# Performance work log

Measured on AMD Instinct MI355X. Metric: run time of the kernel, lower is better.

The kernel has to match this reference:

```python
import jax, jax.numpy as jnp
import numpy as np

INF = 1000000000.0
D = 1024


def setup_inputs() -> dict:
    key = jax.random.key(0)
    k_enc, k_r = jax.random.split(key)
    encoding = jax.random.normal(k_enc, (8, 2048, D), dtype=jnp.float32)
    R = jax.random.normal(k_r, (D, D), dtype=jnp.float32) / D  # init_with_zeros=False
    return {"encoding": encoding, "R": R}


def reference(encoding, R):
    b, n, d = encoding.shape
    # Q = encoding @ R ; scores = Q @ encoding^T  (bilinear relation attention)
    encR = jnp.einsum("bnd,de->bne", encoding, R)          # [b, n, d]
    scores = jnp.einsum("bnd,bmd->bnm", encR, encoding)     # [b, n, n]
    # causal mask: -INF above the diagonal (use_mask=True)
    mask = jnp.where(jnp.tril(jnp.ones((n, n), dtype=bool)), 0.0, -INF).astype(scores.dtype)
    A = jax.nn.softmax(scores + mask, axis=2)               # [b, n, n]
    return jnp.einsum("bnm,bmd->bnd", A, encoding)          # [b, n, d]
```

## Files before the change

kernel.cpp:

```cpp
#include <hip/hip_runtime.h>
#include <hip/hip_bf16.h>


typedef __attribute__((ext_vector_type(4))) float f32x4;
typedef __attribute__((ext_vector_type(4))) unsigned u32x4;
typedef __attribute__((ext_vector_type(8))) __fp16 f16x8;
typedef __attribute__((ext_vector_type(4))) __fp16 f16x4;
typedef __attribute__((ext_vector_type(2))) __fp16 f16x2;

#define MFMA16H(A, B, C) __builtin_amdgcn_mfma_f32_16x16x32_f16(A, B, C, 0, 0, 0)

__device__ __forceinline__ f16x4 cvt4h(f32x4 a) {
    union { f16x4 v; f16x2 h[2]; } r;
    r.h[0] = __builtin_amdgcn_cvt_pkrtz(a[0], a[1]);
    r.h[1] = __builtin_amdgcn_cvt_pkrtz(a[2], a[3]);
    return r.v;
}

__device__ __forceinline__ void gload16(const void* g, void* l) {
    __builtin_amdgcn_global_load_lds(
        (const __attribute__((address_space(1))) unsigned*)g,
        (__attribute__((address_space(3))) unsigned*)l, 16, 0, 0);
}

#define BAR() do { __builtin_amdgcn_sched_barrier(0); \
                   __builtin_amdgcn_s_barrier();      \
                   __builtin_amdgcn_sched_barrier(0); } while (0)

__global__ __launch_bounds__(256) void transpose_cvt_kernel(
    const float* __restrict__ enc, __fp16* __restrict__ encT, __fp16* __restrict__ encH,
    const float* __restrict__ R, __fp16* __restrict__ Rt)
{
    __shared__ __align__(16) char lt[64 * 128];
    const int t = threadIdx.x;
    const int bz = blockIdx.z;
    const bool isR = (bz == 8);
    if (isR && blockIdx.x >= 16) return;
    const int Rr = isR ? 1024 : 2048, C = 1024;
    const float* src = isR ? R : enc;
    __fp16* dstT = isR ? Rt : encT;
    __fp16* dstH = isR ? (__fp16*)nullptr : encH;
    const int r0 = blockIdx.x * 64, c0 = blockIdx.y * 64;
    const size_t so = isR ? 0 : (size_t)bz * Rr * C;
    const int tr = t >> 4;
    const int tc4 = (t & 15) * 4;
#pragma unroll
    for (int p = 0; p < 4; ++p) {
        int rl = tr + 16 * p;
        f32x4 x = *(const f32x4*)(src + so + (size_t)(r0 + rl) * C + c0 + tc4);
        f16x4 h = cvt4h(x);
        if (dstH) *(f16x4*)(dstH + so + (size_t)(r0 + rl) * C + c0 + tc4) = h;
        *(f16x4*)(lt + rl * 128 + ((tc4 * 2) ^ ((rl & 7) << 4))) = h;
    }
    __syncthreads();
#pragma unroll
    for (int p = 0; p < 4; ++p) {
        int dl = tr + 16 * p;
#pragma unroll
        for (int j = 0; j < 4; ++j) {
            int kl = (t & 15) + 16 * j;
            __fp16 v = *(const __fp16*)(lt + kl * 128 + ((dl * 2) ^ ((kl & 7) << 4)));
            dstT[so + (size_t)(c0 + dl) * Rr + r0 + kl] = v;
        }
    }
}

__global__ __launch_bounds__(512, 2) void gemm_qr256(
    const __fp16* __restrict__ encH, const __fp16* __restrict__ Rt,
    __fp16* __restrict__ Qh)
{
    __shared__ __align__(16) char lds[131072];
    const int t = threadIdx.x;
    const int w = t >> 6, l = t & 63;
    const int l15 = l & 15, lg = (l >> 4) & 3;
    const int wr = w >> 2, wc = w & 3;
    const int bm = ((int)blockIdx.x >> 2) * 256;
    const int bn = ((int)blockIdx.x & 3) * 256;
    const __fp16* Ag = encH + (size_t)bm * 1024;
    const __fp16* Bg = Rt + (size_t)bn * 1024;

    const int srow = 32 * w + (l >> 2);
    const int slg = ((l & 3) - ((l >> 3) & 3)) & 3;
    const int slotr = ((l >> 4) + ((l & 15) >> 1)) & 3;

    f32x4 acc[8][4];
#pragma unroll
    for (int i = 0; i < 8; ++i)
#pragma unroll
        for (int j = 0; j < 4; ++j) acc[i][j] = (f32x4){0.f, 0.f, 0.f, 0.f};

    auto stage = [&](int op, int tile, int kh) {
        const __fp16* src = (op ? Bg : Ag) + (size_t)srow * 1024 + tile * 64 + kh * 32 + slg * 8;
        char* dst = lds + (tile & 1) * 65536 + op * 32768 + kh * 16384 + w * 2048;
        gload16(src, dst);
        gload16(src + (size_t)16 * 1024, dst + 1024);
    };
    auto rdA = [&](int buf, int ks, int mf) {
        return *(const f16x8*)(lds + buf * 65536 + ks * 16384
                               + (128 * wr + 16 * mf + l15) * 64 + slotr * 16);
    };
    auto rdB = [&](int buf, int ks, int nf) {
        return *(const f16x8*)(lds + buf * 65536 + 32768 + ks * 16384
                               + (64 * wc + 16 * nf + l15) * 64 + slotr * 16);
    };

    stage(0, 0, 0); stage(1, 0, 0); stage(0, 0, 1); stage(1, 0, 1);
    stage(0, 1, 0); stage(1, 1, 0);

    f16x8 afr[4], bfr[4];

#define MF16(mbase)                                                     \
    __builtin_amdgcn_s_setprio(1);                                      \
    _Pragma("unroll") for (int mf = 0; mf < 4; ++mf)                    \
        _Pragma("unroll") for (int nf = 0; nf < 4; ++nf)                \
            acc[(mbase) + mf][nf] = MFMA16H(afr[mf], bfr[nf], acc[(mbase) + mf][nf]); \
    __builtin_amdgcn_s_setprio(0);

    for (int i = 0; i < 8; ++i) {
        const bool lastI = (i == 7);
        asm volatile("s_waitcnt vmcnt(8)" ::: "memory");
        BAR();
#pragma unroll
        for (int nf = 0; nf < 4; ++nf) bfr[nf] = rdB(0, 0, nf);
#pragma unroll
        for (int mf = 0; mf < 4; ++mf) afr[mf] = rdA(0, 0, mf);
        stage(0, 2 * i + 1, 1);
        MF16(0)
        BAR();
#pragma unroll
        for (int mf = 0; mf < 4; ++mf) afr[mf] = rdA(0, 0, mf + 4);
        stage(1, 2 * i + 1, 1);
        MF16(4)
        asm volatile("s_waitcnt vmcnt(8)" ::: "memory");
        BAR();
#pragma unroll
        for (int nf = 0; nf < 4; ++nf) bfr[nf] = rdB(0, 1, nf);
#pragma unroll
        for (int mf = 0; mf < 4; ++mf) afr[mf] = rdA(0, 1, mf);
        if (!lastI) stage(0, 2 * i + 2, 0);
        MF16(0)
        BAR();
#pragma unroll
        for (int mf = 0; mf < 4; ++mf) afr[mf] = rdA(0, 1, mf + 4);
        if (!lastI) stage(1, 2 * i + 2, 0);
        MF16(4)
        if (!lastI) asm volatile("s_waitcnt vmcnt(8)" ::: "memory");
        else        asm volatile("s_waitcnt vmcnt(4)" ::: "memory");
        BAR();
#pragma unroll
        for (int nf = 0; nf < 4; ++nf) bfr[nf] = rdB(1, 0, nf);
#pragma unroll
        for (int mf = 0; mf < 4; ++mf) afr[mf] = rdA(1, 0, mf);
        if (!lastI) stage(0, 2 * i + 2, 1);
        MF16(0)
        BAR();
#pragma unroll
        for (int mf = 0; mf < 4; ++mf) afr[mf] = rdA(1, 0, mf + 4);
        if (!lastI) stage(1, 2 * i + 2, 1);
        MF16(4)
        if (!lastI) asm volatile("s_waitcnt vmcnt(8)" ::: "memory");
        else        asm volatile("s_waitcnt vmcnt(0)" ::: "memory");
        BAR();
#pragma unroll
        for (int nf = 0; nf < 4; ++nf) bfr[nf] = rdB(1, 1, nf);
#pragma unroll
        for (int mf = 0; mf < 4; ++mf) afr[mf] = rdA(1, 1, mf);
        if (!lastI) stage(0, 2 * i + 3, 0);
        MF16(0)
        BAR();
#pragma unroll
        for (int mf = 0; mf < 4; ++mf) afr[mf] = rdA(1, 1, mf + 4);
        if (!lastI) stage(1, 2 * i + 3, 0);
        MF16(4)
    }
#undef MF16

#pragma unroll
    for (int mf = 0; mf < 8; ++mf)
#pragma unroll
        for (int nf = 0; nf < 4; ++nf)
#pragma unroll
            for (int rg = 0; rg < 4; ++rg) {
                int rr = bm + 128 * wr + 16 * mf + 4 * lg + rg;
                int cc = bn + 64 * wc + 16 * nf + l15;
                Qh[(size_t)rr * 1024 + cc] = (__fp16)acc[mf][nf][rg];
            }
}

template <int CMODE>
__device__ __forceinline__ void core256x128(
    const __fp16* __restrict__ A, int ldA, const __fp16* __restrict__ B, int ldB,
    char* __restrict__ Cptr, int ldC, int K, int rowOff, int colOff, bool maskDiag)
{
    __shared__ __align__(16) char lds[73728];
    const int t = threadIdx.x;
    const int w = t >> 6, l = t & 63;
    const int l15 = l & 15, lg = (l >> 4) & 3;
    const int wr = w >> 1, wc = w & 1;

    const int srowA = 32 * w + (l >> 2);
    const int srowB = 16 * w + (l >> 2);
    const int slg = ((l & 3) - ((l >> 3) & 3)) & 3;
    const int slotr = ((l >> 4) + ((l & 15) >> 1)) & 3;

    f32x4 acc[4][4];
#pragma unroll
    for (int i = 0; i < 4; ++i)
#pragma unroll
        for (int j = 0; j < 4; ++j) acc[i][j] = (f32x4){0.f, 0.f, 0.f, 0.f};
    f32x4 acc_rs[4];
#pragma unroll
    for (int i = 0; i < 4; ++i) acc_rs[i] = (f32x4){0.f, 0.f, 0.f, 0.f};
    f16x8 ones;
#pragma unroll
    for (int j = 0; j < 8; ++j) ones[j] = (__fp16)1.f;

    auto stageH = [&](int h) {
        const int reg = h % 3;
        const __fp16* sa = A + (size_t)srowA * ldA + h * 32 + slg * 8;
        char* da = lds + reg * 16384 + w * 2048;
        gload16(sa, da);
        gload16(sa + (size_t)16 * ldA, da + 1024);
        const __fp16* sb = B + (size_t)srowB * ldB + h * 32 + slg * 8;
        gload16(sb, lds + 49152 + reg * 8192 + w * 1024);
    };
    auto rdA = [&](int h, int mf) {
        return *(const f16x8*)(lds + (h % 3) * 16384
                               + (64 * wr + 16 * mf + l15) * 64 + slotr * 16);
    };
    auto rdB = [&](int h, int nf) {
        return *(const f16x8*)(lds + 49152 + (h % 3) * 8192
                               + (64 * wc + 16 * nf + l15) * 64 + slotr * 16);
    };

    const int nh = K >> 5;
    stageH(0); stageH(1);

    f16x8 afr[4], bfr[4];
    for (int h = 0; h < nh; ++h) {
        if (h + 1 < nh) asm volatile("s_waitcnt vmcnt(3)" ::: "memory");
        else            asm volatile("s_waitcnt vmcnt(0)" ::: "memory");
        BAR();
#pragma unroll
        for (int nf = 0; nf < 4; ++nf) bfr[nf] = rdB(h, nf);
#pragma unroll
        for (int mf = 0; mf < 4; ++mf) afr[mf] = rdA(h, mf);
        if (h + 2 < nh) stageH(h + 2);
        __builtin_amdgcn_s_setprio(1);
#pragma unroll
        for (int mf = 0; mf < 4; ++mf) {
#pragma unroll
            for (int nf = 0; nf < 4; ++nf)
                acc[mf][nf] = MFMA16H(afr[mf], bfr[nf], acc[mf][nf]);
            if (CMODE == 2)
                acc_rs[mf] = MFMA16H(afr[mf], ones, acc_rs[mf]);
        }
        __builtin_amdgcn_s_setprio(0);
    }
    BAR();

    if (CMODE == 1) {
#pragma unroll
        for (int mf = 0; mf < 4; ++mf)
#pragma unroll
            for (int nf = 0; nf < 4; ++nf)
#pragma unroll
                for (int rg = 0; rg < 4; ++rg) {
                    int rr = 64 * wr + 16 * mf + 4 * lg + rg;
                    int cc = 64 * wc + 16 * nf + l15;
                    bool msk = maskDiag && (colOff + cc > rowOff + rr);
                    float e = msk ? 0.f
                                  : __builtin_amdgcn_exp2f(acc[mf][nf][rg] * 1.4426950408889634f);
                    *(__fp16*)(Cptr + ((size_t)rr * ldC + cc) * 2) = (__fp16)e;
                }
    } else {
#pragma unroll
        for (int mf = 0; mf < 4; ++mf)
#pragma unroll
            for (int nf = 0; nf < 4; ++nf)
#pragma unroll
                for (int rg = 0; rg < 4; ++rg) {
                    int rr = 64 * wr + 16 * mf + 4 * lg + rg;
                    int cc = 64 * wc + 16 * nf + l15;
                    *(float*)(Cptr + ((size_t)rr * ldC + cc) * 4) =
                        acc[mf][nf][rg] / acc_rs[mf][rg];
                }
    }
}

__global__ __launch_bounds__(512, 4) void gemm_s256(
    const __fp16* __restrict__ Qh, const __fp16* __restrict__ encH,
    __fp16* __restrict__ S)
{
    const int b = (int)blockIdx.x & 7;
    const int r = (int)blockIdx.x >> 3;
    int qt = 0;
    while (r >= (qt + 1) * (qt + 2)) ++qt;
    const int nt = r - qt * (qt + 1);
    const size_t bo = (size_t)b * 2048 * 1024;
    const size_t so = (size_t)b * 2048 * 2048;
    core256x128<1>(Qh + bo + (size_t)(256 * qt) * 1024, 1024,
                   encH + bo + (size_t)(128 * nt) * 1024, 1024,
                   (char*)(S + so + (size_t)(256 * qt) * 2048 + 128 * nt), 2048,
                   1024, 256 * qt, 128 * nt, (nt >> 1) == qt);
}

__global__ __launch_bounds__(512, 4) void gemm_pv256(
    const __fp16* __restrict__ P, const __fp16* __restrict__ encT,
    float* __restrict__ out)
{
    const int b = (int)blockIdx.x & 7;
    const int r = (int)blockIdx.x >> 3;
    const int qtb = 7 - (r >> 3);
    const int dblk = r & 7;
    const size_t so = (size_t)b * 2048 * 2048;
    const size_t to = (size_t)b * 1024 * 2048;
    const size_t oo = (size_t)b * 2048 * 1024;
    core256x128<2>(P + so + (size_t)(256 * qtb) * 2048, 2048,
                   encT + to + (size_t)(128 * dblk) * 2048, 2048,
                   (char*)(out + oo + (size_t)(256 * qtb) * 1024 + 128 * dblk), 1024,
                   256 * (qtb + 1), 0, 0, false);
}

__global__ __launch_bounds__(256) void softmax_kernel(__fp16* __restrict__ S, int sh)
{
    const int t = threadIdx.x;
    const int wv = t >> 6, l = t & 63;
    const int r = blockIdx.x * 4 + wv;
    const int b = blockIdx.y;
    __fp16* row = S + ((size_t)b * 2048 + r) * 2048;
    const int L = ((r >> sh) + 1) << sh;

    float v[4][8];
    float mx = -1e30f;
#pragma unroll
    for (int i = 0; i < 4; ++i) {
        int c0 = 8 * l + 512 * i;
        if (c0 < L) {
            f16x8 h = *reinterpret_cast<const f16x8*>(row + c0);
#pragma unroll
            for (int j = 0; j < 8; ++j) { v[i][j] = (float)h[j]; mx = fmaxf(mx, v[i][j]); }
        } else {
#pragma unroll
            for (int j = 0; j < 8; ++j) v[i][j] = -1e30f;
        }
    }
#pragma unroll
    for (int off = 1; off < 64; off <<= 1) mx = fmaxf(mx, __shfl_xor(mx, off));
    float sm = 0.f;
#pragma unroll
    for (int i = 0; i < 4; ++i)
#pragma unroll
        for (int j = 0; j < 8; ++j) { v[i][j] = __expf(v[i][j] - mx); sm += v[i][j]; }
#pragma unroll
    for (int off = 1; off < 64; off <<= 1) sm += __shfl_xor(sm, off);
    const float inv = 1.f / sm;
#pragma unroll
    for (int i = 0; i < 4; ++i) {
        int c0 = 8 * l + 512 * i;
        if (c0 < L) {
            union { f16x8 v8; f16x2 h[4]; } o;
#pragma unroll
            for (int j = 0; j < 4; ++j)
                o.h[j] = __builtin_amdgcn_cvt_pkrtz(v[i][2 * j] * inv, v[i][2 * j + 1] * inv);
            *reinterpret_cast<f16x8*>(row + c0) = o.v8;
        }
    }
}

__global__ __launch_bounds__(256) void qr_gemm_kernel(
    const float* __restrict__ A, const float* __restrict__ B, float* C)
{
    __shared__ __align__(16) char sA[128 * 64];
    __shared__ __align__(16) char sB[128 * 64];
    const int t = threadIdx.x;
    const int w = t >> 6, l = t & 63;
    const int l15 = l & 15, lg = l >> 4;
    const int bm = blockIdx.x * 128;
    const int bn = blockIdx.y * 128;

    f32x4 acc[4][4];
#pragma unroll
    for (int i = 0; i < 4; ++i)
#pragma unroll
        for (int j = 0; j < 4; ++j) acc[i][j] = (f32x4){0.f, 0.f, 0.f, 0.f};

    const int kq = 4 * (t & 7);
    const int i2 = t >> 3;

    for (int kk = 0; kk < 1024; kk += 32) {
#pragma unroll
        for (int it = 0; it < 4; ++it) {
            int m = i2 + 32 * it;
            f32x4 x = *reinterpret_cast<const f32x4*>(&A[(size_t)(bm + m) * 1024 + kk + kq]);
            *reinterpret_cast<f16x4*>(sA + m * 64 + ((2 * kq) ^ (((m >> 1) & 3) << 4))) = cvt4h(x);
        }
        {
            int n0 = 4 * i2;
            f32x4 x[4];
#pragma unroll
            for (int r = 0; r < 4; ++r)
                x[r] = *reinterpret_cast<const f32x4*>(&B[(size_t)(kk + kq + r) * 1024 + bn + n0]);
#pragma unroll
            for (int j = 0; j < 4; ++j) {
                int n = n0 + j;
                union { f16x4 v; f16x2 h[2]; } s;
                s.h[0] = __builtin_amdgcn_cvt_pkrtz(x[0][j], x[1][j]);
                s.h[1] = __builtin_amdgcn_cvt_pkrtz(x[2][j], x[3][j]);
                *reinterpret_cast<f16x4*>(sB + n * 64 + ((2 * kq) ^ (((n >> 1) & 3) << 4))) = s.v;
            }
        }
        __syncthreads();
        f16x8 af[4], bfv[4];
        const int r0 = (w >> 1) * 64, c0 = (w & 1) * 64;
#pragma unroll
        for (int mt = 0; mt < 4; ++mt) {
            int m = r0 + 16 * mt + l15;
            af[mt] = *reinterpret_cast<f16x8*>(sA + m * 64 + ((16 * lg) ^ (((m >> 1) & 3) << 4)));
        }
#pragma unroll
        for (int nt = 0; nt < 4; ++nt) {
            int n = c0 + 16 * nt + l15;
            bfv[nt] = *reinterpret_cast<f16x8*>(sB + n * 64 + ((16 * lg) ^ (((n >> 1) & 3) << 4)));
        }
#pragma unroll
        for (int mt = 0; mt < 4; ++mt)
#pragma unroll
            for (int nt = 0; nt < 4; ++nt)
                acc[mt][nt] = MFMA16H(af[mt], bfv[nt], acc[mt][nt]);
        __syncthreads();
    }
#pragma unroll
    for (int mt = 0; mt < 4; ++mt)
#pragma unroll
        for (int nt = 0; nt < 4; ++nt)
#pragma unroll
            for (int rg = 0; rg < 4; ++rg) {
                int row = bm + (w >> 1) * 64 + 16 * mt + 4 * lg + rg;
                int col = bn + (w & 1) * 64 + 16 * nt + l15;
                C[(size_t)row * 1024 + col] = acc[mt][nt][rg];
            }
}

__global__ __launch_bounds__(256) void s_gemm_kernel(
    const float* __restrict__ Q, const float* __restrict__ enc, __fp16* __restrict__ S)
{
    __shared__ __align__(16) char sA[128 * 64];
    __shared__ __align__(16) char sB[128 * 64];
    const int t = threadIdx.x;
    const int w = t >> 6, l = t & 63;
    const int l15 = l & 15, lg = l >> 4;

    int rem = 135 - (int)blockIdx.x;
    int qt = 0;
    while (rem > qt) { rem -= qt + 1; ++qt; }
    const int kt = rem;
    const int b = blockIdx.y;
    const float* Arow = Q + ((size_t)b * 2048 + qt * 128) * 1024;
    const float* Brow = enc + ((size_t)b * 2048 + kt * 128) * 1024;

    f32x4 acc[4][4];
#pragma unroll
    for (int i = 0; i < 4; ++i)
#pragma unroll
        for (int j = 0; j < 4; ++j) acc[i][j] = (f32x4){0.f, 0.f, 0.f, 0.f};

    const int kq = 4 * (t & 7);
    const int i2 = t >> 3;

    for (int kk = 0; kk < 1024; kk += 32) {
#pragma unroll
        for (int it = 0; it < 4; ++it) {
            int m = i2 + 32 * it;
            int sw = (2 * kq) ^ (((m >> 1) & 3) << 4);
            f32x4 xa = *reinterpret_cast<const f32x4*>(&Arow[(size_t)m * 1024 + kk + kq]);
            f32x4 xb = *reinterpret_cast<const f32x4*>(&Brow[(size_t)m * 1024 + kk + kq]);
            *reinterpret_cast<f16x4*>(sA + m * 64 + sw) = cvt4h(xa);
            *reinterpret_cast<f16x4*>(sB + m * 64 + sw) = cvt4h(xb);
        }
        __syncthreads();
        f16x8 af[4], bfv[4];
        const int r0 = (w >> 1) * 64, c0 = (w & 1) * 64;
#pragma unroll
        for (int mt = 0; mt < 4; ++mt) {
            int m = r0 + 16 * mt + l15;
            af[mt] = *reinterpret_cast<f16x8*>(sA + m * 64 + ((16 * lg) ^ (((m >> 1) & 3) << 4)));
        }
#pragma unroll
        for (int nt = 0; nt < 4; ++nt) {
            int n = c0 + 16 * nt + l15;
            bfv[nt] = *reinterpret_cast<f16x8*>(sB + n * 64 + ((16 * lg) ^ (((n >> 1) & 3) << 4)));
        }
#pragma unroll
        for (int mt = 0; mt < 4; ++mt)
#pragma unroll
            for (int nt = 0; nt < 4; ++nt)
                acc[mt][nt] = MFMA16H(af[mt], bfv[nt], acc[mt][nt]);
        __syncthreads();
    }
    const int r0 = (w >> 1) * 64, c0 = (w & 1) * 64;
#pragma unroll
    for (int mt = 0; mt < 4; ++mt)
#pragma unroll
        for (int nt = 0; nt < 4; ++nt)
#pragma unroll
            for (int rg = 0; rg < 4; ++rg) {
                int rt = r0 + 16 * mt + 4 * lg + rg;
                int ct = c0 + 16 * nt + l15;
                float v = acc[mt][nt][rg];
                if (kt == qt && ct > rt) v = -30000.f;
                S[((size_t)b * 2048 + qt * 128 + rt) * 2048 + kt * 128 + ct] = (__fp16)v;
            }
}

__global__ __launch_bounds__(512) void pv_gemm_kernel(
    const __fp16* __restrict__ P, const float* __restrict__ enc, float* __restrict__ out)
{
    __shared__ __align__(16) char sA[128 * 128];
    __shared__ __align__(16) char sB[128 * 128];
    const int t = threadIdx.x;
    const int w = t >> 6, l = t & 63;
    const int l15 = l & 15, lg = (l >> 4) & 3;
    const int wq = w >> 2, wdv = w & 3;
    const int qtb = 15 - (int)blockIdx.x;
    const int dblk = blockIdx.y;
    const int b = blockIdx.z;
    const int q0 = 128 * qtb;
    const int nkv = 128 * (qtb + 1);
    const __fp16* Pbase = P + ((size_t)b * 2048 + q0) * 2048;
    const float* Eb = enc + (size_t)b * 2048 * 1024;

    f32x4 acc[4][2];
#pragma unroll
    for (int i = 0; i < 4; ++i)
#pragma unroll
        for (int j = 0; j < 2; ++j) acc[i][j] = (f32x4){0.f, 0.f, 0.f, 0.f};

    const int ar = t >> 2, aseg = t & 3;
    const int ba = t >> 5, bdq = t & 31;

    for (int kv0 = 0; kv0 < nkv; kv0 += 64) {
        __syncthreads();
        {
            const __fp16* src = Pbase + (size_t)ar * 2048 + kv0 + 16 * aseg;
            u32x4 v0 = *reinterpret_cast<const u32x4*>(src);
            u32x4 v1 = *reinterpret_cast<const u32x4*>(src + 8);
            const int sw = (ar & 7) << 4;
            *reinterpret_cast<u32x4*>(sA + ar * 128 + ((32 * aseg) ^ sw)) = v0;
            *reinterpret_cast<u32x4*>(sA + ar * 128 + ((32 * aseg + 16) ^ sw)) = v1;
        }
        {
            const float* src = Eb + (size_t)(kv0 + 4 * ba) * 1024 + 128 * dblk + 4 * bdq;
            f32x4 x0 = *reinterpret_cast<const f32x4*>(src);
            f32x4 x1 = *reinterpret_cast<const f32x4*>(src + 1024);
            f32x4 x2 = *reinterpret_cast<const f32x4*>(src + 2048);
            f32x4 x3 = *reinterpret_cast<const f32x4*>(src + 3072);
#pragma unroll
            for (int j = 0; j < 4; ++j) {
                int d = 4 * bdq + j;
                union { f16x4 v; f16x2 h[2]; } s;
                s.h[0] = __builtin_amdgcn_cvt_pkrtz(x0[j], x1[j]);
                s.h[1] = __builtin_amdgcn_cvt_pkrtz(x2[j], x3[j]);
                *reinterpret_cast<f16x4*>(sB + d * 128 + ((8 * ba) ^ ((d & 7) << 4))) = s.v;
            }
        }
        __syncthreads();
#pragma unroll
        for (int ks = 0; ks < 2; ++ks) {
            f16x8 afr[4], bfr[2];
#pragma unroll
            for (int mt = 0; mt < 4; ++mt) {
                int rr = 64 * wq + 16 * mt + l15;
                afr[mt] = *reinterpret_cast<f16x8*>(sA + rr * 128 + ((64 * ks + 16 * lg) ^ ((rr & 7) << 4)));
            }
#pragma unroll
            for (int nt = 0; nt < 2; ++nt) {
                int d = 32 * wdv + 16 * nt + l15;
                bfr[nt] = *reinterpret_cast<f16x8*>(sB + d * 128 + ((64 * ks + 16 * lg) ^ ((d & 7) << 4)));
            }
#pragma unroll
            for (int mt = 0; mt < 4; ++mt)
#pragma unroll
                for (int nt = 0; nt < 2; ++nt)
                    acc[mt][nt] = MFMA16H(afr[mt], bfr[nt], acc[mt][nt]);
        }
    }
#pragma unroll
    for (int mt = 0; mt < 4; ++mt)
#pragma unroll
        for (int nt = 0; nt < 2; ++nt)
#pragma unroll
            for (int rg = 0; rg < 4; ++rg) {
                size_t row = (size_t)b * 2048 + q0 + 64 * wq + 16 * mt + 4 * lg + rg;
                int col = 128 * dblk + 32 * wdv + 16 * nt + l15;
                out[row * 1024 + col] = acc[mt][nt][rg];
            }
}

extern "C" void kernel_launch(void* const* d_in, const int* in_sizes, int n_in,
                              void* d_out, int out_size, void* d_ws, size_t ws_size,
                              hipStream_t stream)
{
    const float* enc = (const float*)d_in[0];
    const float* R = (const float*)d_in[1];
    float* out = (float*)d_out;
    const size_t MB = 1u << 20;

    if (ws_size >= 98 * MB) {
        __fp16* S = (__fp16*)d_ws;
        __fp16* encT = (__fp16*)((char*)d_ws + 64 * MB);
        __fp16* Rt = (__fp16*)((char*)d_ws + 96 * MB);
        __fp16* Qh = (__fp16*)d_out;
        __fp16* encH = (__fp16*)d_out + (size_t)16384 * 1024;

        transpose_cvt_kernel<<<dim3(32, 16, 9), 256, 0, stream>>>(enc, encT, encH, R, Rt);
        gemm_qr256<<<dim3(256), 512, 0, stream>>>(encH, Rt, Qh);
        gemm_s256<<<dim3(576), 512, 0, stream>>>(Qh, encH, S);
        gemm_pv256<<<dim3(512), 512, 0, stream>>>(S, encT, out);
    } else {
        __fp16* S = (__fp16*)d_ws;
        qr_gemm_kernel<<<dim3(128, 8), 256, 0, stream>>>(enc, R, out);
        s_gemm_kernel<<<dim3(136, 8), 256, 0, stream>>>(out, enc, S);
        softmax_kernel<<<dim3(512, 8), 256, 0, stream>>>(S, 7);
        pv_gemm_kernel<<<dim3(16, 8, 8), 512, 0, stream>>>(S, enc, out);
    }
}
```

Before: 170.5 us.

## Compute causal score GEMM with 256x256 tiles reusing QR GEMM core

Generalizes the 256x256 QR GEMM core into a templated routine with an optional exp-and-causal-mask epilogue, and uses it for the score GEMM. The score kernel switches from 256x128 tiles (576 blocks) to square 256x256 lower-triangular tiles (288 blocks). This raises arithmetic intensity per tile and cuts redundant loads of Q. The cost is fewer blocks, lower occupancy (2 blocks per CU instead of 4), and more masked work on the diagonal tiles.

```diff
diff --git a/kernel.cpp b/kernel.cpp
--- a/kernel.cpp
+++ b/kernel.cpp
@@ -65,19 +65,16 @@
     }
 }
 
-__global__ __launch_bounds__(512, 2) void gemm_qr256(
-    const __fp16* __restrict__ encH, const __fp16* __restrict__ Rt,
-    __fp16* __restrict__ Qh)
+template <int CMODE>
+__device__ __forceinline__ void core256sq(
+    const __fp16* __restrict__ Ag, const __fp16* __restrict__ Bg,
+    __fp16* __restrict__ Cbase, int ldC, bool diag)
 {
     __shared__ __align__(16) char lds[131072];
     const int t = threadIdx.x;
     const int w = t >> 6, l = t & 63;
     const int l15 = l & 15, lg = (l >> 4) & 3;
     const int wr = w >> 2, wc = w & 3;
-    const int bm = ((int)blockIdx.x >> 2) * 256;
-    const int bn = ((int)blockIdx.x & 3) * 256;
-    const __fp16* Ag = encH + (size_t)bm * 1024;
-    const __fp16* Bg = Rt + (size_t)bn * 1024;
 
     const int srow = 32 * w + (l >> 2);
     const int slg = ((l & 3) - ((l >> 3) & 3)) & 3;
@@ -181,16 +178,46 @@
         for (int nf = 0; nf < 4; ++nf)
 #pragma unroll
             for (int rg = 0; rg < 4; ++rg) {
-                int rr = bm + 128 * wr + 16 * mf + 4 * lg + rg;
-                int cc = bn + 64 * wc + 16 * nf + l15;
-                Qh[(size_t)rr * 1024 + cc] = (__fp16)acc[mf][nf][rg];
-            }
-}
-
-template <int CMODE>
-__device__ __forceinline__ void core256x128(
+                int rr = 128 * wr + 16 * mf + 4 * lg + rg;
+                int cc = 64 * wc + 16 * nf + l15;
+                float v = acc[mf][nf][rg];
+                if (CMODE == 1) {
+                    bool msk = diag && (cc > rr);
+                    v = msk ? 0.f : __builtin_amdgcn_exp2f(v * 1.4426950408889634f);
+                }
+                Cbase[(size_t)rr * ldC + cc] = (__fp16)v;
+            }
+}
+
+__global__ __launch_bounds__(512, 2) void gemm_qr256(
+    const __fp16* __restrict__ encH, const __fp16* __restrict__ Rt,
+    __fp16* __restrict__ Qh)
+{
+    const int bm = ((int)blockIdx.x >> 2) * 256;
+    const int bn = ((int)blockIdx.x & 3) * 256;
+    core256sq<0>(encH + (size_t)bm * 1024, Rt + (size_t)bn * 1024,
+                 Qh + (size_t)bm * 1024 + bn, 1024, false);
+}
+
+__global__ __launch_bounds__(512, 2) void gemm_s256sq(
+    const __fp16* __restrict__ Qh, const __fp16* __restrict__ encH,
+    __fp16* __restrict__ S)
+{
+    const int b = (int)blockIdx.x & 7;
+    const int r = (int)blockIdx.x >> 3;
+    int qt = 0;
+    while (r >= ((qt + 1) * (qt + 2)) / 2) ++qt;
+    const int nt = r - (qt * (qt + 1)) / 2;
+    const size_t bo = (size_t)b * 2048 * 1024;
+    const size_t so = (size_t)b * 2048 * 2048;
+    core256sq<1>(Qh + bo + (size_t)(256 * qt) * 1024,
+                 encH + bo + (size_t)(256 * nt) * 1024,
+                 S + so + (size_t)(256 * qt) * 2048 + 256 * nt, 2048, nt == qt);
+}
+
+__device__ __forceinline__ void core256x128_pv(
     const __fp16* __restrict__ A, int ldA, const __fp16* __restrict__ B, int ldB,
-    char* __restrict__ Cptr, int ldC, int K, int rowOff, int colOff, bool maskDiag)
+    float* __restrict__ Cptr, int ldC, int K)
 {
     __shared__ __align__(16) char lds[73728];
     const int t = threadIdx.x;
@@ -252,57 +279,22 @@
 #pragma unroll
             for (int nf = 0; nf < 4; ++nf)
                 acc[mf][nf] = MFMA16H(afr[mf], bfr[nf], acc[mf][nf]);
-            if (CMODE == 2)
-                acc_rs[mf] = MFMA16H(afr[mf], ones, acc_rs[mf]);
+            acc_rs[mf] = MFMA16H(afr[mf], ones, acc_rs[mf]);
         }
         __builtin_amdgcn_s_setprio(0);
     }
     BAR();
 
-    if (CMODE == 1) {
-#pragma unroll
-        for (int mf = 0; mf < 4; ++mf)
-#pragma unroll
-            for (int nf = 0; nf < 4; ++nf)
-#pragma unroll
-                for (int rg = 0; rg < 4; ++rg) {
-                    int rr = 64 * wr + 16 * mf + 4 * lg + rg;
-                    int cc = 64 * wc + 16 * nf + l15;
-                    bool msk = maskDiag && (colOff + cc > rowOff + rr);
-                    float e = msk ? 0.f
-                                  : __builtin_amdgcn_exp2f(acc[mf][nf][rg] * 1.4426950408889634f);
-                    *(__fp16*)(Cptr + ((size_t)rr * ldC + cc) * 2) = (__fp16)e;
-                }
-    } else {
-#pragma unroll
-        for (int mf = 0; mf < 4; ++mf)
-#pragma unroll
-            for (int nf = 0; nf < 4; ++nf)
-#pragma unroll
-                for (int rg = 0; rg < 4; ++rg) {
-                    int rr = 64 * wr + 16 * mf + 4 * lg + rg;
-                    int cc = 64 * wc + 16 * nf + l15;
-                    *(float*)(Cptr + ((size_t)rr * ldC + cc) * 4) =
-                        acc[mf][nf][rg] / acc_rs[mf][rg];
-                }
-    }
-}
-
-__global__ __launch_bounds__(512, 4) void gemm_s256(
-    const __fp16* __restrict__ Qh, const __fp16* __restrict__ encH,
-    __fp16* __restrict__ S)
-{
-    const int b = (int)blockIdx.x & 7;
-    const int r = (int)blockIdx.x >> 3;
-    int qt = 0;
-    while (r >= (qt + 1) * (qt + 2)) ++qt;
-    const int nt = r - qt * (qt + 1);
-    const size_t bo = (size_t)b * 2048 * 1024;
-    const size_t so = (size_t)b * 2048 * 2048;
-    core256x128<1>(Qh + bo + (size_t)(256 * qt) * 1024, 1024,
-                   encH + bo + (size_t)(128 * nt) * 1024, 1024,
-                   (char*)(S + so + (size_t)(256 * qt) * 2048 + 128 * nt), 2048,
-                   1024, 256 * qt, 128 * nt, (nt >> 1) == qt);
+#pragma unroll
+    for (int mf = 0; mf < 4; ++mf)
+#pragma unroll
+        for (int nf = 0; nf < 4; ++nf)
+#pragma unroll
+            for (int rg = 0; rg < 4; ++rg) {
+                int rr = 64 * wr + 16 * mf + 4 * lg + rg;
+                int cc = 64 * wc + 16 * nf + l15;
+                Cptr[(size_t)rr * ldC + cc] = acc[mf][nf][rg] / acc_rs[mf][rg];
+            }
 }
 
 __global__ __launch_bounds__(512, 4) void gemm_pv256(
@@ -316,10 +308,10 @@
     const size_t so = (size_t)b * 2048 * 2048;
     const size_t to = (size_t)b * 1024 * 2048;
     const size_t oo = (size_t)b * 2048 * 1024;
-    core256x128<2>(P + so + (size_t)(256 * qtb) * 2048, 2048,
+    core256x128_pv(P + so + (size_t)(256 * qtb) * 2048, 2048,
                    encT + to + (size_t)(128 * dblk) * 2048, 2048,
-                   (char*)(out + oo + (size_t)(256 * qtb) * 1024 + 128 * dblk), 1024,
-                   256 * (qtb + 1), 0, 0, false);
+                   out + oo + (size_t)(256 * qtb) * 1024 + 128 * dblk, 1024,
+                   256 * (qtb + 1));
 }
 
 __global__ __launch_bounds__(256) void softmax_kernel(__fp16* __restrict__ S, int sh)
@@ -615,7 +607,7 @@
 
         transpose_cvt_kernel<<<dim3(32, 16, 9), 256, 0, stream>>>(enc, encT, encH, R, Rt);
         gemm_qr256<<<dim3(256), 512, 0, stream>>>(encH, Rt, Qh);
-        gemm_s256<<<dim3(576), 512, 0, stream>>>(Qh, encH, S);
+        gemm_s256sq<<<dim3(288), 512, 0, stream>>>(Qh, encH, S);
         gemm_pv256<<<dim3(512), 512, 0, stream>>>(S, encT, out);
     } else {
         __fp16* S = (__fp16*)d_ws;
```

New measurement: 178.5 us. 1.05x slower.
